# Kernel tuning notes

Hardware: AMD Instinct MI355X
Metric: run time of the kernel (lower is better)

The kernel has to match this reference:

```python
import jax, jax.numpy as jnp
import numpy as np

N_NODES = 50000
N_EDGES = 800000
HIDDEN = 128


def setup_inputs() -> dict:
    key = jax.random.key(0)
    ks = jax.random.split(key, 8)
    z = jax.random.normal(ks[0], (N_NODES, HIDDEN), dtype=jnp.float32)
    weights = jax.random.normal(ks[1], (N_EDGES, 1), dtype=jnp.float32)
    sources = jax.random.randint(ks[2], (N_EDGES,), 0, N_NODES)
    dests = jax.random.randint(ks[3], (N_EDGES,), 0, N_NODES)
    # Linear params (stored [in, out]); scale ~ 1/sqrt(fan_in) like torch default
    in_m = 2 * HIDDEN + 1
    in_u = 2 * HIDDEN
    Wm = jax.random.uniform(ks[4], (in_m, HIDDEN), dtype=jnp.float32, minval=-1.0, maxval=1.0) / np.sqrt(in_m)
    bm = jax.random.uniform(ks[5], (HIDDEN,), dtype=jnp.float32, minval=-1.0, maxval=1.0) / np.sqrt(in_m)
    Wu = jax.random.uniform(ks[6], (in_u, HIDDEN), dtype=jnp.float32, minval=-1.0, maxval=1.0) / np.sqrt(in_u)
    bu = jax.random.uniform(ks[7], (HIDDEN,), dtype=jnp.float32, minval=-1.0, maxval=1.0) / np.sqrt(in_u)
    return {"z": z, "weights": weights, "sources": sources, "dests": dests,
            "Wm": Wm, "bm": bm, "Wu": Wu, "bu": bu}


def reference(z, weights, sources, dests, Wm, bm, Wu, bu):
    n = z.shape[0]
    # gather + concat message input: [E, 2d+1]
    inp = jnp.concatenate([z[dests], z[sources], weights], axis=1)
    messages = inp @ Wm + bm                      # [E, d]
    # scatter_reduce amax over destination nodes; empty segments -> -inf
    m = jax.ops.segment_max(messages, dests, num_segments=n)
    m = jnp.where(jnp.isneginf(m), jnp.zeros_like(m), m)
    h = jnp.concatenate([z, m], axis=1) @ Wu + bu  # [N, d]
    return h
```

## Files before the change

### kernel.cpp

```cpp
#include <hip/hip_runtime.h>
#include <math.h>

#define HIDDEN 128
#define PAD_DEG 64
#define NPART 8
#define CHUNK 2048

typedef __attribute__((ext_vector_type(8))) _Float16 f16x8;
typedef __attribute__((ext_vector_type(4))) float f32x4;
typedef __attribute__((ext_vector_type(2))) _Float16 h2;

__device__ inline unsigned short f2h(float x) {
    _Float16 h = (_Float16)x;
    return __builtin_bit_cast(unsigned short, h);
}
__device__ inline float h2f(unsigned short u) {
    return (float)__builtin_bit_cast(_Float16, u);
}
__device__ inline float h2f_lo(unsigned int u) { return h2f((unsigned short)(u & 0xffff)); }
__device__ inline float h2f_hi(unsigned int u) { return h2f((unsigned short)(u >> 16)); }
__device__ inline h2 hmax2(h2 a, h2 b) {
    h2 r;
    r[0] = a[0] > b[0] ? a[0] : b[0];
    r[1] = a[1] > b[1] ? a[1] : b[1];
    return r;
}

__global__ void prep_kernel(const float* __restrict__ Wm, const float* __restrict__ Wu,
                            const float* __restrict__ bm, const float* __restrict__ bu,
                            unsigned short* __restrict__ WmT0, unsigned short* __restrict__ WmT1,
                            unsigned short* __restrict__ WuT_fold, float* __restrict__ bfold,
                            float* __restrict__ wlast, int* __restrict__ counts, int n) {
    int t = blockIdx.x * blockDim.x + threadIdx.x;
    if (t < 16384) {
        int nn = t >> 7, k = t & 127;
        WmT0[t] = f2h(Wm[k * 128 + nn]);
    } else if (t < 32768) {
        int s = t - 16384;
        int nn = s >> 7, k = s & 127;
        WmT1[s] = f2h(Wm[(128 + k) * 128 + nn]);
    } else if (t < 49152) {
        int s = t - 32768;
        int nn = s >> 7, k = s & 127;
        WuT_fold[nn * 256 + 128 + k] = f2h(Wu[(128 + k) * 128 + nn]);
    } else if (t < 65536) {
        int s = t - 49152;
        int k = s >> 7, nn = s & 127;
        float acc = Wu[k * 128 + nn];
        for (int j = 0; j < 128; ++j)
            acc = fmaf(Wm[k * 128 + j], Wu[(128 + j) * 128 + nn], acc);
        WuT_fold[nn * 256 + k] = f2h(acc);
    } else if (t < 65664) {
        int i = t - 65536;
        wlast[i] = Wm[256 * 128 + i];
    } else if (t < 65792) {
        int i = t - 65664;
        float acc = bu[i];
        for (int k = 0; k < 128; ++k)
            acc = fmaf(bm[k], Wu[(128 + k) * 128 + i], acc);
        bfold[i] = acc;
    } else if (t < 65792 + n) {
        counts[t - 65792] = 0;
    }
}

__global__ __launch_bounds__(256) void gemm_msg(const float* __restrict__ Z,
                                                const unsigned short* __restrict__ WmT1,
                                                unsigned short* __restrict__ P2h,
                                                int n) {
    __shared__ unsigned short As[64][136];
    __shared__ unsigned short Bs[128][136];

    const int m0 = blockIdx.x * 64;
    const int tid = threadIdx.x;
    const int wave = tid >> 6, lane = tid & 63;
    const int l15 = lane & 15, q = lane >> 4;
    const int wrow = wave * 16;

#pragma unroll
    for (int i = 0; i < 4; ++i) {
        int f = tid + i * 256;
        int row = f >> 4, c8 = f & 15;
        int gr = min(m0 + row, n - 1);
        const float4* src = (const float4*)&Z[(size_t)gr * 128 + c8 * 8];
        float4 a = src[0], b = src[1];
        f16x8 hv;
        hv[0] = (_Float16)a.x; hv[1] = (_Float16)a.y; hv[2] = (_Float16)a.z; hv[3] = (_Float16)a.w;
        hv[4] = (_Float16)b.x; hv[5] = (_Float16)b.y; hv[6] = (_Float16)b.z; hv[7] = (_Float16)b.w;
        *(f16x8*)&As[row][c8 * 8] = hv;
    }
#pragma unroll
    for (int i = 0; i < 8; ++i) {
        int f = tid + i * 256;
        int row = f >> 4, c4 = f & 15;
        *(float4*)&Bs[row][c4 * 8] = ((const float4*)WmT1)[row * 16 + c4];
    }
    __syncthreads();

    f32x4 acc[8];
#pragma unroll
    for (int nt = 0; nt < 8; ++nt) acc[nt] = (f32x4){0.f, 0.f, 0.f, 0.f};

#pragma unroll
    for (int ks = 0; ks < 4; ++ks) {
        int k0 = ks * 32;
        f16x8 a = *(const f16x8*)&As[wrow + l15][k0 + q * 8];
#pragma unroll
        for (int nt = 0; nt < 8; ++nt) {
            f16x8 b = *(const f16x8*)&Bs[nt * 16 + l15][k0 + q * 8];
            acc[nt] = __builtin_amdgcn_mfma_f32_16x16x32_f16(a, b, acc[nt], 0, 0, 0);
        }
    }

#pragma unroll
    for (int nt = 0; nt < 8; ++nt) {
#pragma unroll
        for (int r = 0; r < 4; ++r) {
            int row = m0 + wrow + q * 4 + r;
            if (row < n) P2h[(size_t)row * 128 + nt * 16 + l15] = f2h(acc[nt][r]);
        }
    }
}

__global__ __launch_bounds__(256) void scatter_part(const int* __restrict__ dests,
                                                    const int* __restrict__ sources,
                                                    const float* __restrict__ weights,
                                                    int* __restrict__ counts,
                                                    unsigned int* __restrict__ edge_pk,
                                                    int E, int span, int n) {
    const int part = blockIdx.x & (NPART - 1);
    const int chunk = blockIdx.x >> 3;
    const int lo = part * span;
    const int hi = min(lo + span, n);
    const int base = chunk * CHUNK;

#pragma unroll
    for (int i = 0; i < CHUNK; i += 256) {
        int e = base + i + threadIdx.x;
        if (e < E) {
            int d = dests[e];
            if (d >= lo && d < hi) {
                int pos = atomicAdd(&counts[d], 1);
                if (pos < PAD_DEG) {
                    unsigned int pk = (unsigned int)(sources[e] & 0xffff) |
                                      ((unsigned int)f2h(weights[e]) << 16);
                    edge_pk[(size_t)d * PAD_DEG + pos] = pk;
                }
            }
        }
    }
}

__global__ __launch_bounds__(256) void segmax_kernel(const float* __restrict__ Z,
                                                     const unsigned short* __restrict__ P2h,
                                                     const int* __restrict__ counts,
                                                     const unsigned int* __restrict__ edge_pk,
                                                     const float* __restrict__ wlast,
                                                     const unsigned short* __restrict__ WmT0,
                                                     const float* __restrict__ bm,
                                                     unsigned short* __restrict__ Sh, int n) {
    const int wave = threadIdx.x >> 6;
    const int lane = threadIdx.x & 63;
    const int v = blockIdx.x * 4 + wave;
    if (v >= n) return;

    const int l16 = lane & 15;
    const int e4 = lane >> 4;
    const uint4* P2q = (const uint4*)P2h;
    const int cnt = min(counts[v], PAD_DEG);

    int pk = (lane < cnt) ? (int)edge_pk[(size_t)v * PAD_DEG + lane] : 0;

    float4 wfa = ((const float4*)wlast)[l16 * 2];
    float4 wfb = ((const float4*)wlast)[l16 * 2 + 1];
    h2 wl0, wl1, wl2, wl3;
    wl0[0] = (_Float16)wfa.x; wl0[1] = (_Float16)wfa.y;
    wl1[0] = (_Float16)wfa.z; wl1[1] = (_Float16)wfa.w;
    wl2[0] = (_Float16)wfb.x; wl2[1] = (_Float16)wfb.y;
    wl3[0] = (_Float16)wfb.z; wl3[1] = (_Float16)wfb.w;

    const h2 NEGINF = __builtin_bit_cast(h2, 0xFC00FC00u);
    h2 a0 = NEGINF, a1 = NEGINF, a2 = NEGINF, a3 = NEGINF;

    int j = 0;
    for (; j + 8 <= cnt; j += 8) {
        unsigned int pa = (unsigned int)__shfl(pk, j + e4);
        unsigned int pb = (unsigned int)__shfl(pk, j + 4 + e4);
        int sa = pa & 0xffff, sb = pb & 0xffff;
        uint4 ua = P2q[(size_t)sa * 16 + l16];
        uint4 ub = P2q[(size_t)sb * 16 + l16];
        h2 wva = __builtin_bit_cast(h2, (pa & 0xffff0000u) | (pa >> 16));
        h2 wvb = __builtin_bit_cast(h2, (pb & 0xffff0000u) | (pb >> 16));
        a0 = hmax2(a0, wva * wl0 + __builtin_bit_cast(h2, ua.x));
        a1 = hmax2(a1, wva * wl1 + __builtin_bit_cast(h2, ua.y));
        a2 = hmax2(a2, wva * wl2 + __builtin_bit_cast(h2, ua.z));
        a3 = hmax2(a3, wva * wl3 + __builtin_bit_cast(h2, ua.w));
        a0 = hmax2(a0, wvb * wl0 + __builtin_bit_cast(h2, ub.x));
        a1 = hmax2(a1, wvb * wl1 + __builtin_bit_cast(h2, ub.y));
        a2 = hmax2(a2, wvb * wl2 + __builtin_bit_cast(h2, ub.z));
        a3 = hmax2(a3, wvb * wl3 + __builtin_bit_cast(h2, ub.w));
    }
    for (; j < cnt; j += 4) {
        int idx = j + e4;
        bool valid = idx < cnt;
        unsigned int pa = (unsigned int)__shfl(pk, valid ? idx : 0);
        if (valid) {
            int sa = pa & 0xffff;
            uint4 ua = P2q[(size_t)sa * 16 + l16];
            h2 wva = __builtin_bit_cast(h2, (pa & 0xffff0000u) | (pa >> 16));
            a0 = hmax2(a0, wva * wl0 + __builtin_bit_cast(h2, ua.x));
            a1 = hmax2(a1, wva * wl1 + __builtin_bit_cast(h2, ua.y));
            a2 = hmax2(a2, wva * wl2 + __builtin_bit_cast(h2, ua.z));
            a3 = hmax2(a3, wva * wl3 + __builtin_bit_cast(h2, ua.w));
        }
    }

    a0 = hmax2(a0, __builtin_bit_cast(h2, __shfl_xor(__builtin_bit_cast(int, a0), 16)));
    a1 = hmax2(a1, __builtin_bit_cast(h2, __shfl_xor(__builtin_bit_cast(int, a1), 16)));
    a2 = hmax2(a2, __builtin_bit_cast(h2, __shfl_xor(__builtin_bit_cast(int, a2), 16)));
    a3 = hmax2(a3, __builtin_bit_cast(h2, __shfl_xor(__builtin_bit_cast(int, a3), 16)));
    a0 = hmax2(a0, __builtin_bit_cast(h2, __shfl_xor(__builtin_bit_cast(int, a0), 32)));
    a1 = hmax2(a1, __builtin_bit_cast(h2, __shfl_xor(__builtin_bit_cast(int, a1), 32)));
    a2 = hmax2(a2, __builtin_bit_cast(h2, __shfl_xor(__builtin_bit_cast(int, a2), 32)));
    a3 = hmax2(a3, __builtin_bit_cast(h2, __shfl_xor(__builtin_bit_cast(int, a3), 32)));

    if (e4 == 0) {
        uint4 o;
        if (cnt > 0) {
            o.x = __builtin_bit_cast(unsigned int, a0);
            o.y = __builtin_bit_cast(unsigned int, a1);
            o.z = __builtin_bit_cast(unsigned int, a2);
            o.w = __builtin_bit_cast(unsigned int, a3);
        } else {
            float s[8];
#pragma unroll
            for (int d = 0; d < 8; ++d) s[d] = bm[l16 * 8 + d];
            for (int k = 0; k < 128; ++k) {
                float zk = Z[(size_t)v * 128 + k];
#pragma unroll
                for (int d = 0; d < 8; ++d)
                    s[d] = fmaf(zk, h2f(WmT0[(l16 * 8 + d) * 128 + k]), s[d]);
            }
            o.x = (unsigned int)f2h(-s[0]) | ((unsigned int)f2h(-s[1]) << 16);
            o.y = (unsigned int)f2h(-s[2]) | ((unsigned int)f2h(-s[3]) << 16);
            o.z = (unsigned int)f2h(-s[4]) | ((unsigned int)f2h(-s[5]) << 16);
            o.w = (unsigned int)f2h(-s[6]) | ((unsigned int)f2h(-s[7]) << 16);
        }
        ((uint4*)Sh)[(size_t)v * 16 + l16] = o;
    }
}

__global__ __launch_bounds__(256) void gemm_out(const float* __restrict__ Z,
                                                const unsigned short* __restrict__ Sh,
                                                const unsigned short* __restrict__ WuT_fold,
                                                const float* __restrict__ bfold,
                                                float* __restrict__ H, int n) {
    __shared__ unsigned short As[64][136];
    __shared__ unsigned short Bs[128][136];

    const int m0 = blockIdx.x * 64;
    const int tid = threadIdx.x;
    const int wave = tid >> 6, lane = tid & 63;
    const int l15 = lane & 15, q = lane >> 4;
    const int wrow = wave * 16;

    f32x4 acc[8];
#pragma unroll
    for (int nt = 0; nt < 8; ++nt) acc[nt] = (f32x4){0.f, 0.f, 0.f, 0.f};

    for (int h = 0; h < 2; ++h) {
#pragma unroll
        for (int i = 0; i < 8; ++i) {
            int f = tid + i * 256;
            int row = f >> 4, c4 = f & 15;
            *(float4*)&Bs[row][c4 * 8] = ((const float4*)WuT_fold)[row * 32 + h * 16 + c4];
        }
        if (h == 0) {
#pragma unroll
            for (int i = 0; i < 4; ++i) {
                int f = tid + i * 256;
                int row = f >> 4, c8 = f & 15;
                int gr = min(m0 + row, n - 1);
                const float4* src = (const float4*)&Z[(size_t)gr * 128 + c8 * 8];
                float4 a = src[0], b = src[1];
                f16x8 hv;
                hv[0] = (_Float16)a.x; hv[1] = (_Float16)a.y; hv[2] = (_Float16)a.z; hv[3] = (_Float16)a.w;
                hv[4] = (_Float16)b.x; hv[5] = (_Float16)b.y; hv[6] = (_Float16)b.z; hv[7] = (_Float16)b.w;
                *(f16x8*)&As[row][c8 * 8] = hv;
            }
        } else {
#pragma unroll
            for (int i = 0; i < 4; ++i) {
                int f = tid + i * 256;
                int row = f >> 4, c4 = f & 15;
                int gr = min(m0 + row, n - 1);
                *(float4*)&As[row][c4 * 8] = ((const float4*)&Sh[(size_t)gr * 128])[c4];
            }
        }
        __syncthreads();

#pragma unroll
        for (int ks = 0; ks < 4; ++ks) {
            int k0 = ks * 32;
            f16x8 a = *(const f16x8*)&As[wrow + l15][k0 + q * 8];
#pragma unroll
            for (int nt = 0; nt < 8; ++nt) {
                f16x8 b = *(const f16x8*)&Bs[nt * 16 + l15][k0 + q * 8];
                acc[nt] = __builtin_amdgcn_mfma_f32_16x16x32_f16(a, b, acc[nt], 0, 0, 0);
            }
        }
        __syncthreads();
    }

#pragma unroll
    for (int nt = 0; nt < 8; ++nt) {
        int col = nt * 16 + l15;
        float bias = bfold[col];
#pragma unroll
        for (int r = 0; r < 4; ++r) {
            int row = m0 + wrow + q * 4 + r;
            if (row < n) H[(size_t)row * 128 + col] = acc[nt][r] + bias;
        }
    }
}

extern "C" void kernel_launch(void* const* d_in, const int* in_sizes, int n_in,
                              void* d_out, int out_size, void* d_ws, size_t ws_size,
                              hipStream_t stream) {
    const float* z = (const float*)d_in[0];
    const float* weights = (const float*)d_in[1];
    const int* sources = (const int*)d_in[2];
    const int* dests = (const int*)d_in[3];
    const float* Wm = (const float*)d_in[4];
    const float* bm = (const float*)d_in[5];
    const float* Wu = (const float*)d_in[6];
    const float* bu = (const float*)d_in[7];

    const int n = in_sizes[0] / HIDDEN;
    const int E = in_sizes[1];
    float* H = (float*)d_out;

    char* w = (char*)d_ws;
    auto alloc = [&](size_t bytes) { void* p = w; w += (bytes + 255) & ~(size_t)255; return p; };
    unsigned short* Sh  = (unsigned short*)alloc((size_t)n * 128 * 2);
    unsigned short* WmT0 = (unsigned short*)alloc(16384 * 2);
    unsigned short* WmT1 = (unsigned short*)alloc(16384 * 2);
    unsigned short* WuT_fold = (unsigned short*)alloc(32768 * 2);
    float* bfold = (float*)alloc(128 * 4);
    float* wlast = (float*)alloc(128 * 4);
    int* counts  = (int*)alloc((size_t)n * 4);
    unsigned int* edge_pk = (unsigned int*)alloc((size_t)n * PAD_DEG * 4);

    unsigned short* P2h = (unsigned short*)d_out;

    const int mblocks = (n + 63) / 64;
    const int prep_threads = 65792 + n;
    const int span = (n + NPART - 1) / NPART;
    const int nchunks = (E + CHUNK - 1) / CHUNK;

    prep_kernel<<<(prep_threads + 255) / 256, 256, 0, stream>>>(Wm, Wu, bm, bu, WmT0, WmT1,
                                                                WuT_fold, bfold, wlast, counts, n);
    gemm_msg<<<mblocks, 256, 0, stream>>>(z, WmT1, P2h, n);
    scatter_part<<<nchunks * NPART, 256, 0, stream>>>(dests, sources, weights, counts,
                                                      edge_pk, E, span, n);
    segmax_kernel<<<(n + 3) / 4, 256, 0, stream>>>(z, P2h, counts, edge_pk,
                                                   wlast, WmT0, bm, Sh, n);
    gemm_out<<<mblocks, 256, 0, stream>>>(z, Sh, WuT_fold, bfold, H, n);
}
```

Before: 191.5 us.

## Fuse message GEMM and edge scatter into one launch with XCC-aware work stealing

```diff
diff --git a/kernel.cpp b/kernel.cpp
--- a/kernel.cpp
+++ b/kernel.cpp
@@ -5,6 +5,7 @@
 #define PAD_DEG 64
 #define NPART 8
 #define CHUNK 2048
+#define NSCAT 2048
 
 typedef __attribute__((ext_vector_type(8))) _Float16 f16x8;
 typedef __attribute__((ext_vector_type(4))) float f32x4;
@@ -30,7 +31,8 @@
                             const float* __restrict__ bm, const float* __restrict__ bu,
                             unsigned short* __restrict__ WmT0, unsigned short* __restrict__ WmT1,
                             unsigned short* __restrict__ WuT_fold, float* __restrict__ bfold,
-                            float* __restrict__ wlast, int* __restrict__ counts, int n) {
+                            float* __restrict__ wlast, int* __restrict__ counts,
+                            int* __restrict__ ccur, int n) {
     int t = blockIdx.x * blockDim.x + threadIdx.x;
     if (t < 16384) {
         int nn = t >> 7, k = t & 127;
@@ -61,90 +63,88 @@
         bfold[i] = acc;
     } else if (t < 65792 + n) {
         counts[t - 65792] = 0;
-    }
-}
-
-__global__ __launch_bounds__(256) void gemm_msg(const float* __restrict__ Z,
-                                                const unsigned short* __restrict__ WmT1,
-                                                unsigned short* __restrict__ P2h,
-                                                int n) {
-    __shared__ unsigned short As[64][136];
-    __shared__ unsigned short Bs[128][136];
-
-    const int m0 = blockIdx.x * 64;
+    } else if (t < 65792 + n + NPART) {
+        ccur[t - 65792 - n] = 0;
+    }
+}
+
+__global__ __launch_bounds__(256) void fused_msg_scatter(
+        const float* __restrict__ Z,
+        const unsigned short* __restrict__ WmT1,
+        unsigned short* __restrict__ P2h,
+        const int* __restrict__ dests,
+        const int* __restrict__ sources,
+        const float* __restrict__ weights,
+        int* __restrict__ counts,
+        unsigned int* __restrict__ edge_pk,
+        int* __restrict__ ccur,
+        int n, int E, int span, int nchunks, int gblocks) {
     const int tid = threadIdx.x;
-    const int wave = tid >> 6, lane = tid & 63;
-    const int l15 = lane & 15, q = lane >> 4;
-    const int wrow = wave * 16;
-
-#pragma unroll
-    for (int i = 0; i < 4; ++i) {
-        int f = tid + i * 256;
-        int row = f >> 4, c8 = f & 15;
-        int gr = min(m0 + row, n - 1);
-        const float4* src = (const float4*)&Z[(size_t)gr * 128 + c8 * 8];
-        float4 a = src[0], b = src[1];
-        f16x8 hv;
-        hv[0] = (_Float16)a.x; hv[1] = (_Float16)a.y; hv[2] = (_Float16)a.z; hv[3] = (_Float16)a.w;
-        hv[4] = (_Float16)b.x; hv[5] = (_Float16)b.y; hv[6] = (_Float16)b.z; hv[7] = (_Float16)b.w;
-        *(f16x8*)&As[row][c8 * 8] = hv;
-    }
-#pragma unroll
-    for (int i = 0; i < 8; ++i) {
-        int f = tid + i * 256;
-        int row = f >> 4, c4 = f & 15;
-        *(float4*)&Bs[row][c4 * 8] = ((const float4*)WmT1)[row * 16 + c4];
-    }
-    __syncthreads();
-
-    f32x4 acc[8];
-#pragma unroll
-    for (int nt = 0; nt < 8; ++nt) acc[nt] = (f32x4){0.f, 0.f, 0.f, 0.f};
-
-#pragma unroll
-    for (int ks = 0; ks < 4; ++ks) {
-        int k0 = ks * 32;
-        f16x8 a = *(const f16x8*)&As[wrow + l15][k0 + q * 8];
+
+    if ((int)blockIdx.x < gblocks) {
+        const int m0 = blockIdx.x * 64;
+        const int wave = tid >> 6, lane = tid & 63;
+        const int l15 = lane & 15, q = lane >> 4;
+        const int row_a = min(m0 + wave * 16 + l15, n - 1);
+
+        f32x4 acc[8];
+#pragma unroll
+        for (int nt = 0; nt < 8; ++nt) acc[nt] = (f32x4){0.f, 0.f, 0.f, 0.f};
+
+#pragma unroll
+        for (int ks = 0; ks < 4; ++ks) {
+            int k0 = ks * 32;
+            const float4* zp = (const float4*)&Z[(size_t)row_a * 128 + k0 + q * 8];
+            float4 z0 = zp[0], z1 = zp[1];
+            f16x8 a;
+            a[0] = (_Float16)z0.x; a[1] = (_Float16)z0.y;
+            a[2] = (_Float16)z0.z; a[3] = (_Float16)z0.w;
+            a[4] = (_Float16)z1.x; a[5] = (_Float16)z1.y;
+            a[6] = (_Float16)z1.z; a[7] = (_Float16)z1.w;
+#pragma unroll
+            for (int nt = 0; nt < 8; ++nt) {
+                f16x8 b = *(const f16x8*)&WmT1[(size_t)(nt * 16 + l15) * 128 + k0 + q * 8];
+                acc[nt] = __builtin_amdgcn_mfma_f32_16x16x32_f16(a, b, acc[nt], 0, 0, 0);
+            }
+        }
+
 #pragma unroll
         for (int nt = 0; nt < 8; ++nt) {
-            f16x8 b = *(const f16x8*)&Bs[nt * 16 + l15][k0 + q * 8];
-            acc[nt] = __builtin_amdgcn_mfma_f32_16x16x32_f16(a, b, acc[nt], 0, 0, 0);
-        }
-    }
-
-#pragma unroll
-    for (int nt = 0; nt < 8; ++nt) {
-#pragma unroll
-        for (int r = 0; r < 4; ++r) {
-            int row = m0 + wrow + q * 4 + r;
-            if (row < n) P2h[(size_t)row * 128 + nt * 16 + l15] = f2h(acc[nt][r]);
-        }
-    }
-}
-
-__global__ __launch_bounds__(256) void scatter_part(const int* __restrict__ dests,
-                                                    const int* __restrict__ sources,
-                                                    const float* __restrict__ weights,
-                                                    int* __restrict__ counts,
-                                                    unsigned int* __restrict__ edge_pk,
-                                                    int E, int span, int n) {
-    const int part = blockIdx.x & (NPART - 1);
-    const int chunk = blockIdx.x >> 3;
-    const int lo = part * span;
-    const int hi = min(lo + span, n);
-    const int base = chunk * CHUNK;
-
-#pragma unroll
-    for (int i = 0; i < CHUNK; i += 256) {
-        int e = base + i + threadIdx.x;
-        if (e < E) {
-            int d = dests[e];
-            if (d >= lo && d < hi) {
-                int pos = atomicAdd(&counts[d], 1);
-                if (pos < PAD_DEG) {
-                    unsigned int pk = (unsigned int)(sources[e] & 0xffff) |
-                                      ((unsigned int)f2h(weights[e]) << 16);
-                    edge_pk[(size_t)d * PAD_DEG + pos] = pk;
+#pragma unroll
+            for (int r = 0; r < 4; ++r) {
+                int row = m0 + wave * 16 + q * 4 + r;
+                if (row < n) P2h[(size_t)row * 128 + nt * 16 + l15] = f2h(acc[nt][r]);
+            }
+        }
+    } else {
+        __shared__ int c_sh;
+        const int xcc = __builtin_amdgcn_s_getreg(6164) & (NPART - 1);
+
+        for (int t8 = 0; t8 < NPART; ++t8) {
+            const int p = (xcc + t8) & (NPART - 1);
+            const int lo = p * span;
+            const int hi = min(lo + span, n);
+            for (;;) {
+                if (tid == 0) c_sh = atomicAdd(&ccur[p], 1);
+                __syncthreads();
+                const int c = c_sh;
+                __syncthreads();
+                if (c >= nchunks) break;
+                const int base = c * CHUNK;
+#pragma unroll
+                for (int i = 0; i < CHUNK; i += 256) {
+                    int e = base + i + tid;
+                    if (e < E) {
+                        int d = dests[e];
+                        if (d >= lo && d < hi) {
+                            int pos = atomicAdd(&counts[d], 1);
+                            if (pos < PAD_DEG) {
+                                unsigned int pk = (unsigned int)(sources[e] & 0xffff) |
+                                                  ((unsigned int)f2h(weights[e]) << 16);
+                                edge_pk[(size_t)d * PAD_DEG + pos] = pk;
+                            }
+                        }
+                    }
                 }
             }
         }
@@ -349,20 +349,22 @@
     float* bfold = (float*)alloc(128 * 4);
     float* wlast = (float*)alloc(128 * 4);
     int* counts  = (int*)alloc((size_t)n * 4);
+    int* ccur    = (int*)alloc(NPART * 4);
     unsigned int* edge_pk = (unsigned int*)alloc((size_t)n * PAD_DEG * 4);
 
     unsigned short* P2h = (unsigned short*)d_out;
 
     const int mblocks = (n + 63) / 64;
-    const int prep_threads = 65792 + n;
+    const int prep_threads = 65792 + n + NPART;
     const int span = (n + NPART - 1) / NPART;
     const int nchunks = (E + CHUNK - 1) / CHUNK;
 
     prep_kernel<<<(prep_threads + 255) / 256, 256, 0, stream>>>(Wm, Wu, bm, bu, WmT0, WmT1,
-                                                                WuT_fold, bfold, wlast, counts, n);
-    gemm_msg<<<mblocks, 256, 0, stream>>>(z, WmT1, P2h, n);
-    scatter_part<<<nchunks * NPART, 256, 0, stream>>>(dests, sources, weights, counts,
-                                                      edge_pk, E, span, n);
+                                                                WuT_fold, bfold, wlast,
+                                                                counts, ccur, n);
+    fused_msg_scatter<<<mblocks + NSCAT, 256, 0, stream>>>(
+        z, WmT1, P2h, dests, sources, weights, counts, edge_pk, ccur,
+        n, E, span, nchunks, mblocks);
     segmax_kernel<<<(n + 3) / 4, 256, 0, stream>>>(z, P2h, counts, edge_pk,
                                                    wlast, WmT0, bm, Sh, n);
     gemm_out<<<mblocks, 256, 0, stream>>>(z, Sh, WuT_fold, bfold, H, n);
```

New measurement: 380.6 us. 1.99x slower.
